# Performance work log

Measured on AMD Instinct MI355X. Metric: run time of the kernel, lower is better.

## Reference

```python
import jax, jax.numpy as jnp
import numpy as np

N = 100000; E = 1600000; D_IN = 9; HID = 16; HEADS = 8; D = HID * HEADS; G = 1000
NEG_SLOPE = 0.2; LN_EPS = 1e-5


def _gat_conv(x, src, dst, W, a_src, a_dst, b, heads, ch):
    # PyG GATConv (eval mode, self-loops already appended to src/dst)
    h = (x @ W).reshape(-1, heads, ch)                   # [N,H,C]
    al_s = (h * a_src).sum(-1)                           # [N,H]
    al_d = (h * a_dst).sum(-1)                           # [N,H]
    e = al_s[src] + al_d[dst]                            # [Et,H]
    e = jnp.where(e > 0, e, NEG_SLOPE * e)               # LeakyReLU(0.2)
    m = jax.ops.segment_max(e, dst, num_segments=N)      # per-dst softmax
    alpha = jnp.exp(e - m[dst])
    denom = jax.ops.segment_sum(alpha, dst, num_segments=N)
    alpha = alpha / (denom[dst] + 1e-16)
    out = jax.ops.segment_sum(h[src] * alpha[:, :, None], dst, num_segments=N)
    return out.reshape(-1, heads * ch) + b


def _ln_graph(x, g, b):
    # PyG LayerNorm, mode='graph', batch=None: normalize over all nodes+channels
    mu = x.mean()
    var = jnp.mean((x - mu) ** 2)
    return (x - mu) / jnp.sqrt(var + LN_EPS) * g + b


def setup_inputs() -> dict:
    key = jax.random.key(0)
    ks = jax.random.split(key, 20)
    s = 0.1
    p = lambda i, shape: jax.random.normal(ks[i], shape, jnp.float32) * s
    return {
        "x": jax.random.normal(ks[0], (N, D_IN), jnp.float32),
        "edge_index": jax.random.randint(ks[1], (2, E), 0, N),
        "batch": jnp.sort(jax.random.randint(ks[2], (N,), 0, G)),
        "W1": p(3, (D_IN, D)), "a_src1": p(4, (HEADS, HID)), "a_dst1": p(5, (HEADS, HID)), "b1": jnp.zeros((D,), jnp.float32),
        "W2": p(6, (D, D)), "a_src2": p(7, (1, D)), "a_dst2": p(8, (1, D)), "b2": jnp.zeros((D,), jnp.float32),
        "fc1_w": p(9, (D, D)), "fc1_b": jnp.zeros((D,), jnp.float32),
        "fc2_w": p(10, (D, D)), "fc2_b": jnp.zeros((D,), jnp.float32),
        "fc3_w": p(11, (D, D)), "fc3_b": jnp.zeros((D,), jnp.float32),
        "fc4_w": p(12, (D, D)), "fc4_b": jnp.zeros((D,), jnp.float32),
        "g1": jnp.ones((D,), jnp.float32), "beta1": jnp.zeros((D,), jnp.float32),
        "g2": jnp.ones((D,), jnp.float32), "beta2": jnp.zeros((D,), jnp.float32),
        "fcf_w": p(13, (D, 1)), "fcf_b": jnp.zeros((1,), jnp.float32),
    }


def reference(x, edge_index, batch, W1, a_src1, a_dst1, b1, W2, a_src2, a_dst2, b2,
              fc1_w, fc1_b, fc2_w, fc2_b, fc3_w, fc3_b, fc4_w, fc4_b,
              g1, beta1, g2, beta2, fcf_w, fcf_b):
    loops = jnp.arange(N)
    src = jnp.concatenate([edge_index[0], loops])
    dst = jnp.concatenate([edge_index[1], loops])
    h = jax.nn.relu(_gat_conv(x, src, dst, W1, a_src1, a_dst1, b1, HEADS, HID))
    hc = h
    h = jax.nn.relu(h @ fc1_w + fc1_b)
    h = jax.nn.relu(h @ fc2_w + fc2_b + hc)
    h = _ln_graph(h, g1, beta1)
    hc = h
    h = _gat_conv(h, src, dst, W2, a_src2, a_dst2, b2, 1, D)
    h = jax.nn.relu(h @ fc3_w + fc3_b)
    h = h @ fc4_w + fc4_b + hc
    h = _ln_graph(h, g2, beta2)
    h = h @ fcf_w + fcf_b                                # [N,1]
    sums = jax.ops.segment_sum(h, batch, num_segments=G)
    cnt = jax.ops.segment_sum(jnp.ones((N,), h.dtype), batch, num_segments=G)
    return sums / jnp.maximum(cnt, 1.0)[:, None]          # global_mean_pool -> [G,1]
```

## Files before the change

kernel.cpp:

```cpp
#include <hip/hip_runtime.h>
#include <cstdint>

#define NN 100000
#define NE 1600000
#define DI 9
#define DD 128
#define NH 8
#define NG 1000

#define NBK 3125
#define NBLK 256
#define EPB (NE/NBLK)

typedef unsigned int uint;
typedef __attribute__((ext_vector_type(8))) short bf16x8;
typedef __attribute__((ext_vector_type(4))) float f32x4;

__device__ __forceinline__ float leaky(float x){ return x > 0.f ? x : 0.2f*x; }
__device__ __forceinline__ uint f2bf(float f){
  uint u = __float_as_uint(f);
  return (u + 0x7fffu + ((u>>16)&1u)) >> 16;
}
__device__ __forceinline__ float bflo(uint p){ return __uint_as_float(p << 16); }
__device__ __forceinline__ float bfhi(uint p){ return __uint_as_float(p & 0xffff0000u); }
__device__ __forceinline__ uint packbf(float a, float b){ return f2bf(a) | (f2bf(b)<<16); }

union U16 { uint4 u; bf16x8 v; };
__device__ __forceinline__ bf16x8 ld8(const uint* p){ U16 t; t.u = *(const uint4*)p; return t.v; }

__global__ __launch_bounds__(512) void k_hist(const int* __restrict__ dst, int* __restrict__ hist){
  __shared__ int h[NBK];
  for (int i = threadIdx.x; i < NBK; i += 512) h[i] = 0;
  __syncthreads();
  int blk = blockIdx.x;
  int beg = blk*EPB, end = beg + EPB;
  for (int i = beg + threadIdx.x; i < end; i += 512)
    atomicAdd(&h[dst[i] >> 5], 1);
  __syncthreads();
  for (int b = threadIdx.x; b < NBK; b += 512) hist[(size_t)blk*NBK + b] = h[b];
}

__global__ __launch_bounds__(256) void k_bsum(int* __restrict__ hist, int* __restrict__ bsum){
  int b = blockIdx.x*256 + threadIdx.x;
  if (b >= NBK) return;
  int run = 0;
  for (int k = 0; k < NBLK; ++k){
    int t = hist[(size_t)k*NBK + b];
    hist[(size_t)k*NBK + b] = run;
    run += t;
  }
  bsum[b] = run;
}

__global__ __launch_bounds__(1024) void k_bscan(const int* __restrict__ bsum, int* __restrict__ bbase){
  __shared__ int sh[1024];
  __shared__ int carry;
  if (threadIdx.x == 0) carry = 0;
  __syncthreads();
  for (int c0 = 0; c0 < NBK; c0 += 1024){
    int i = c0 + threadIdx.x;
    int v = (i < NBK) ? bsum[i] : 0;
    sh[threadIdx.x] = v;
    __syncthreads();
    for (int off = 1; off < 1024; off <<= 1){
      int t = (threadIdx.x >= off) ? sh[threadIdx.x-off] : 0;
      __syncthreads();
      sh[threadIdx.x] += t;
      __syncthreads();
    }
    if (i < NBK) bbase[i] = carry + sh[threadIdx.x] - v;
    __syncthreads();
    if (threadIdx.x == 0) carry += sh[1023];
    __syncthreads();
  }
}

__global__ __launch_bounds__(512) void k_part(const int* __restrict__ src, const int* __restrict__ dst,
    const int* __restrict__ hist, const int* __restrict__ bbase, uint* __restrict__ ebuf){
  __shared__ int cur[NBK];
  int blk = blockIdx.x;
  for (int b = threadIdx.x; b < NBK; b += 512)
    cur[b] = hist[(size_t)blk*NBK + b] + bbase[b];
  __syncthreads();
  int beg = blk*EPB, end = beg + EPB;
  for (int i = beg + threadIdx.x; i < end; i += 512){
    int d = dst[i], s = src[i];
    int b = d >> 5;
    int p = atomicAdd(&cur[b], 1);
    ebuf[p] = (uint)s | ((uint)(d & 31) << 26);
  }
}

__global__ __launch_bounds__(64) void k_fin(const uint* __restrict__ ebuf, const int* __restrict__ bbase,
    const int* __restrict__ bsum, int* __restrict__ rowptr, int* __restrict__ col){
  __shared__ int cnt32[32];
  __shared__ int exc[32];
  int b = blockIdx.x;
  int lane = threadIdx.x;
  if (lane < 32) cnt32[lane] = 0;
  __syncthreads();
  int base = bbase[b], n = bsum[b];
  for (int i = lane; i < n; i += 64)
    atomicAdd(&cnt32[ebuf[base+i] >> 26], 1);
  __syncthreads();
  if (lane == 0){
    int run = 0;
    for (int d = 0; d < 32; ++d){
      int t = cnt32[d];
      exc[d] = run;
      rowptr[b*32 + d] = base + run;
      run += t;
    }
  }
  __syncthreads();
  if (lane < 32) cnt32[lane] = exc[lane];
  __syncthreads();
  for (int i = lane; i < n; i += 64){
    uint e = ebuf[base+i];
    int d = e >> 26;
    int r = atomicAdd(&cnt32[d], 1);
    col[base + r] = (int)(e & 0x03ffffffu);
  }
  if (b == 0 && lane == 0) rowptr[NN] = NE;
}

__global__ __launch_bounds__(64) void k_wconv(const float* __restrict__ W, uint* __restrict__ WT){
  int n = blockIdx.x;
  int t = threadIdx.x;
  float w0 = W[(2*t)*DD + n];
  float w1 = W[(2*t+1)*DD + n];
  WT[n*64 + t] = packbf(w0, w1);
}

__global__ __launch_bounds__(128) void k_lin1(const float* __restrict__ x, const float* __restrict__ W1,
    const float* __restrict__ as1, const float* __restrict__ ad1,
    uint* __restrict__ t1b, float* __restrict__ al_s, float* __restrict__ al_d){
  int n = blockIdx.x;
  int c = threadIdx.x;
  const float* xr = x + n*DI;
  float t = 0.f;
  #pragma unroll
  for (int k = 0; k < DI; ++k) t = fmaf(xr[k], W1[k*DD+c], t);
  uint mybf = f2bf(t);
  uint pbf  = (uint)__shfl_xor((int)mybf, 1, 64);
  if (!(c & 1)) t1b[(size_t)n*64 + (c>>1)] = mybf | (pbf<<16);
  float vs = t * as1[c];
  float vd = t * ad1[c];
  #pragma unroll
  for (int m = 8; m >= 1; m >>= 1){ vs += __shfl_xor(vs, m, 16); vd += __shfl_xor(vd, m, 16); }
  if ((c & 15) == 0){
    al_s[n*NH + (c>>4)] = vs;
    al_d[n*NH + (c>>4)] = vd;
  }
}

__global__ __launch_bounds__(256) void k_gat1(const uint* __restrict__ t1b,
    const float* __restrict__ al_s, const float* __restrict__ al_d,
    const int* __restrict__ rowptr, const int* __restrict__ col,
    const float* __restrict__ b1, uint* __restrict__ outb){
  int n = blockIdx.x*4 + (threadIdx.x >> 6);
  if (n >= NN) return;
  uint lane = threadIdx.x & 63;
  uint h = lane >> 3;
  float ald = al_d[(uint)n*NH + h];
  float a0  = __expf(leaky(al_s[(uint)n*NH + h] + ald));
  uint  ps  = t1b[(uint)n*64u + lane];
  float den = a0;
  float s0 = a0*bflo(ps), s1 = a0*bfhi(ps);
  int beg = rowptr[n], end = rowptr[n+1];
  int e = beg;
  for (; e + 4 <= end; e += 4){
    uint c0 = (uint)col[e], c1 = (uint)col[e+1], c2 = (uint)col[e+2], c3 = (uint)col[e+3];
    float l0 = al_s[c0*8u + h], l1 = al_s[c1*8u + h];
    float l2 = al_s[c2*8u + h], l3 = al_s[c3*8u + h];
    uint p0 = t1b[c0*64u + lane];
    uint p1 = t1b[c1*64u + lane];
    uint p2 = t1b[c2*64u + lane];
    uint p3 = t1b[c3*64u + lane];
    float a0_ = __expf(leaky(l0 + ald));
    float a1_ = __expf(leaky(l1 + ald));
    float a2_ = __expf(leaky(l2 + ald));
    float a3_ = __expf(leaky(l3 + ald));
    den += a0_ + a1_ + a2_ + a3_;
    s0 = fmaf(a0_, bflo(p0), s0); s1 = fmaf(a0_, bfhi(p0), s1);
    s0 = fmaf(a1_, bflo(p1), s0); s1 = fmaf(a1_, bfhi(p1), s1);
    s0 = fmaf(a2_, bflo(p2), s0); s1 = fmaf(a2_, bfhi(p2), s1);
    s0 = fmaf(a3_, bflo(p3), s0); s1 = fmaf(a3_, bfhi(p3), s1);
  }
  for (; e < end; ++e){
    uint c = (uint)col[e];
    float a = __expf(leaky(al_s[c*8u + h] + ald));
    uint p = t1b[c*64u + lane];
    den += a;
    s0 = fmaf(a, bflo(p), s0); s1 = fmaf(a, bfhi(p), s1);
  }
  float inv = 1.f/(den + 1e-16f);
  float2 bb = ((const float2*)b1)[lane];
  outb[(uint)n*64u + lane] = packbf(fmaxf(s0*inv + bb.x, 0.f), fmaxf(s1*inv + bb.y, 0.f));
}

__global__ __launch_bounds__(256) void k_al2(const uint* __restrict__ t2b,
    const float* __restrict__ as2, const float* __restrict__ ad2,
    float* __restrict__ al_s, float* __restrict__ al_d){
  int n = blockIdx.x*4 + (threadIdx.x >> 6);
  if (n >= NN) return;
  int lane = threadIdx.x & 63;
  uint p = t2b[(size_t)n*64 + lane];
  float v0 = bflo(p), v1 = bfhi(p);
  float2 s2 = ((const float2*)as2)[lane];
  float2 d2 = ((const float2*)ad2)[lane];
  float vs = v0*s2.x + v1*s2.y;
  float vd = v0*d2.x + v1*d2.y;
  #pragma unroll
  for (int m = 32; m >= 1; m >>= 1){ vs += __shfl_xor(vs, m, 64); vd += __shfl_xor(vd, m, 64); }
  if (lane == 0){ al_s[n] = vs; al_d[n] = vd; }
}

__global__ __launch_bounds__(256) void k_gat2(const uint* __restrict__ t2b,
    const float* __restrict__ al_s, const float* __restrict__ al_d,
    const int* __restrict__ rowptr, const int* __restrict__ col,
    const float* __restrict__ b2, uint* __restrict__ outb){
  int n = blockIdx.x*4 + (threadIdx.x >> 6);
  if (n >= NN) return;
  uint lane = threadIdx.x & 63;
  float ald = al_d[n];
  float a0  = __expf(leaky(al_s[n] + ald));
  uint  ps  = t2b[(uint)n*64u + lane];
  float den = a0;
  float s0 = a0*bflo(ps), s1 = a0*bfhi(ps);
  int beg = rowptr[n], end = rowptr[n+1];
  int e = beg;
  for (; e + 4 <= end; e += 4){
    uint c0 = (uint)col[e], c1 = (uint)col[e+1], c2 = (uint)col[e+2], c3 = (uint)col[e+3];
    float l0 = al_s[c0], l1 = al_s[c1], l2 = al_s[c2], l3 = al_s[c3];
    uint p0 = t2b[c0*64u + lane];
    uint p1 = t2b[c1*64u + lane];
    uint p2 = t2b[c2*64u + lane];
    uint p3 = t2b[c3*64u + lane];
    float a0_ = __expf(leaky(l0 + ald));
    float a1_ = __expf(leaky(l1 + ald));
    float a2_ = __expf(leaky(l2 + ald));
    float a3_ = __expf(leaky(l3 + ald));
    den += a0_ + a1_ + a2_ + a3_;
    s0 = fmaf(a0_, bflo(p0), s0); s1 = fmaf(a0_, bfhi(p0), s1);
    s0 = fmaf(a1_, bflo(p1), s0); s1 = fmaf(a1_, bfhi(p1), s1);
    s0 = fmaf(a2_, bflo(p2), s0); s1 = fmaf(a2_, bfhi(p2), s1);
    s0 = fmaf(a3_, bflo(p3), s0); s1 = fmaf(a3_, bfhi(p3), s1);
  }
  for (; e < end; ++e){
    uint c = (uint)col[e];
    float a = __expf(leaky(al_s[c] + ald));
    uint p = t2b[c*64u + lane];
    den += a;
    s0 = fmaf(a, bflo(p), s0); s1 = fmaf(a, bfhi(p), s1);
  }
  float inv = 1.f/(den + 1e-16f);
  float2 bb = ((const float2*)b2)[lane];
  outb[(uint)n*64u + lane] = packbf(s0*inv + bb.x, s1*inv + bb.y);
}

template<bool RELU, bool BIAS, bool RES, bool LNRED>
__global__ __launch_bounds__(256) void k_mfma(const uint* __restrict__ Xb, const uint* __restrict__ WTb,
    const float* __restrict__ bias, const uint* __restrict__ resb, uint* __restrict__ outb,
    float* __restrict__ pbuf, int nrows){
  int lane = threadIdx.x & 63;
  int wid  = threadIdx.x >> 6;
  int m0 = blockIdx.x*128 + wid*32;
  int lr = lane & 15, hi4 = lane >> 4;
  f32x4 acc[2][8];
  #pragma unroll
  for (int a = 0; a < 2; ++a)
    #pragma unroll
    for (int c = 0; c < 8; ++c) acc[a][c] = (f32x4){0.f,0.f,0.f,0.f};
  int ra0 = m0 + lr;      if (ra0 > NN-1) ra0 = NN-1;
  int ra1 = m0 + 16 + lr; if (ra1 > NN-1) ra1 = NN-1;
  #pragma unroll
  for (int kk = 0; kk < 4; ++kk){
    int ko = kk*16 + hi4*4;
    bf16x8 a0 = ld8(Xb + (size_t)ra0*64 + ko);
    bf16x8 a1 = ld8(Xb + (size_t)ra1*64 + ko);
    #pragma unroll
    for (int c = 0; c < 8; ++c){
      bf16x8 b = ld8(WTb + (size_t)(c*16 + lr)*64 + ko);
      acc[0][c] = __builtin_amdgcn_mfma_f32_16x16x32_bf16(a0, b, acc[0][c], 0, 0, 0);
      acc[1][c] = __builtin_amdgcn_mfma_f32_16x16x32_bf16(a1, b, acc[1][c], 0, 0, 0);
    }
  }
  bool evn = !(lane & 1);
  int cph = lr >> 1;
  float lns = 0.f, lnss = 0.f;
  #pragma unroll
  for (int rg = 0; rg < 2; ++rg){
    #pragma unroll
    for (int c = 0; c < 8; ++c){
      int cp = c*8 + cph;
      #pragma unroll
      for (int r = 0; r < 4; ++r){
        float v0 = acc[rg][c][r];
        float v1 = __shfl_xor(v0, 1, 64);
        int row = m0 + rg*16 + hi4*4 + r;
        if (evn && row < nrows){
          if (BIAS){ float2 bb = ((const float2*)bias)[cp]; v0 += bb.x; v1 += bb.y; }
          if (RES){ uint rr = resb[(size_t)row*64 + cp]; v0 += bflo(rr); v1 += bfhi(rr); }
          if (RELU){ v0 = fmaxf(v0, 0.f); v1 = fmaxf(v1, 0.f); }
          outb[(size_t)row*64 + cp] = packbf(v0, v1);
          if (LNRED){ lns += v0 + v1; lnss += v0*v0 + v1*v1; }
        }
      }
    }
  }
  if (LNRED){
    #pragma unroll
    for (int m = 32; m >= 1; m >>= 1){ lns += __shfl_xor(lns, m, 64); lnss += __shfl_xor(lnss, m, 64); }
    __shared__ float shred[8];
    if (lane == 0){ shred[wid*2] = lns; shred[wid*2+1] = lnss; }
    __syncthreads();
    if (threadIdx.x == 0){
      float S = 0.f, SS = 0.f;
      for (int w = 0; w < 4; ++w){ S += shred[2*w]; SS += shred[2*w+1]; }
      pbuf[blockIdx.x*2] = S; pbuf[blockIdx.x*2+1] = SS;
    }
  }
}

__global__ __launch_bounds__(256) void k_ln_stats(const float* __restrict__ pbuf, float* __restrict__ stats, int nb){
  float s = 0.f, ss = 0.f;
  for (int i = threadIdx.x; i < nb; i += 256){ s += pbuf[2*i]; ss += pbuf[2*i+1]; }
  #pragma unroll
  for (int m = 32; m >= 1; m >>= 1){ s += __shfl_xor(s, m, 64); ss += __shfl_xor(ss, m, 64); }
  __shared__ float sh[8];
  int wid = threadIdx.x >> 6, lane = threadIdx.x & 63;
  if (lane == 0){ sh[wid*2] = s; sh[wid*2+1] = ss; }
  __syncthreads();
  if (threadIdx.x == 0){
    float S = 0.f, SS = 0.f;
    for (int w = 0; w < 4; ++w){ S += sh[2*w]; SS += sh[2*w+1]; }
    const float inv = 1.f/((float)NN*(float)DD);
    float mu = S*inv;
    float var = SS*inv - mu*mu;
    stats[0] = mu;
    stats[1] = rsqrtf(var + 1e-5f);
  }
}

__global__ __launch_bounds__(256) void k_ln_apply_bf(uint* __restrict__ xb, const float* __restrict__ g,
    const float* __restrict__ be, const float* __restrict__ stats){
  const int n4 = NN*16;
  float mu = stats[0], rs = stats[1];
  uint4* x4 = (uint4*)xb;
  const float2* g2 = (const float2*)g;
  const float2* b2 = (const float2*)be;
  for (int i = blockIdx.x*256 + threadIdx.x; i < n4; i += gridDim.x*256){
    int cb = (i & 15)*4;
    uint4 u = x4[i];
    float2 ga = g2[cb],   gb = g2[cb+1], gc = g2[cb+2], gd = g2[cb+3];
    float2 ba = b2[cb],   bb = b2[cb+1], bc = b2[cb+2], bd = b2[cb+3];
    u.x = packbf((bflo(u.x)-mu)*rs*ga.x + ba.x, (bfhi(u.x)-mu)*rs*ga.y + ba.y);
    u.y = packbf((bflo(u.y)-mu)*rs*gb.x + bb.x, (bfhi(u.y)-mu)*rs*gb.y + bb.y);
    u.z = packbf((bflo(u.z)-mu)*rs*gc.x + bc.x, (bfhi(u.z)-mu)*rs*gc.y + bc.y);
    u.w = packbf((bflo(u.w)-mu)*rs*gd.x + bd.x, (bfhi(u.w)-mu)*rs*gd.y + bd.y);
    x4[i] = u;
  }
}

__global__ __launch_bounds__(256) void k_fdot_ln(const uint* __restrict__ xb, const float* __restrict__ g,
    const float* __restrict__ be, const float* __restrict__ stats,
    const float* __restrict__ fw, const float* __restrict__ fb, float* __restrict__ val){
  int n = blockIdx.x*4 + (threadIdx.x >> 6);
  if (n >= NN) return;
  int lane = threadIdx.x & 63;
  float mu = stats[0], rs = stats[1];
  uint p = xb[(size_t)n*64 + lane];
  float2 gg = ((const float2*)g)[lane];
  float2 bb = ((const float2*)be)[lane];
  float2 ww = ((const float2*)fw)[lane];
  float v = ((bflo(p)-mu)*rs*gg.x + bb.x)*ww.x + ((bfhi(p)-mu)*rs*gg.y + bb.y)*ww.y;
  #pragma unroll
  for (int m = 32; m >= 1; m >>= 1) v += __shfl_xor(v, m, 64);
  if (lane == 0) val[n] = v + fb[0];
}

__global__ __launch_bounds__(64) void k_pool(const float* __restrict__ val, const int* __restrict__ batch,
                                             float* __restrict__ out){
  int g = blockIdx.x;
  int lane = threadIdx.x;
  int lo = 0, hi = NN;
  while (lo < hi){ int mid = (lo+hi)>>1; if (batch[mid] < g) lo = mid+1; else hi = mid; }
  int start = lo;
  hi = NN;
  while (lo < hi){ int mid = (lo+hi)>>1; if (batch[mid] < g+1) lo = mid+1; else hi = mid; }
  int end = lo;
  float s = 0.f;
  for (int i = start + lane; i < end; i += 64) s += val[i];
  #pragma unroll
  for (int m = 32; m >= 1; m >>= 1) s += __shfl_xor(s, m, 64);
  if (lane == 0) out[g] = s / fmaxf((float)(end - start), 1.f);
}

extern "C" void kernel_launch(void* const* d_in, const int* in_sizes, int n_in,
                              void* d_out, int out_size, void* d_ws, size_t ws_size,
                              hipStream_t stream){
  const float* x   = (const float*)d_in[0];
  const int*   ei  = (const int*)d_in[1];
  const int* batch = (const int*)d_in[2];
  const float* W1  = (const float*)d_in[3];
  const float* as1 = (const float*)d_in[4];
  const float* ad1 = (const float*)d_in[5];
  const float* b1  = (const float*)d_in[6];
  const float* W2  = (const float*)d_in[7];
  const float* as2 = (const float*)d_in[8];
  const float* ad2 = (const float*)d_in[9];
  const float* b2  = (const float*)d_in[10];
  const float* fc1w= (const float*)d_in[11];
  const float* fc1b= (const float*)d_in[12];
  const float* fc2w= (const float*)d_in[13];
  const float* fc2b= (const float*)d_in[14];
  const float* fc3w= (const float*)d_in[15];
  const float* fc3b= (const float*)d_in[16];
  const float* fc4w= (const float*)d_in[17];
  const float* fc4b= (const float*)d_in[18];
  const float* g1  = (const float*)d_in[19];
  const float* be1 = (const float*)d_in[20];
  const float* g2  = (const float*)d_in[21];
  const float* be2 = (const float*)d_in[22];
  const float* fcw = (const float*)d_in[23];
  const float* fcb = (const float*)d_in[24];
  float* out = (float*)d_out;
  (void)in_sizes; (void)n_in; (void)out_size; (void)ws_size;

  char* ws = (char*)d_ws;
  size_t off = 0;
  auto alloc = [&](size_t bytes)->void*{
    void* p = ws + off;
    off += (bytes + 255) & ~(size_t)255;
    return p;
  };
  float* A    = (float*)alloc((size_t)NN*DD*4);
  float* B    = (float*)alloc((size_t)NN*DD*4);
  float* C    = (float*)alloc((size_t)NN*DD*4);
  float* als1 = (float*)alloc((size_t)NN*NH*4);
  float* ald1 = (float*)alloc((size_t)NN*NH*4);
  float* als2 = (float*)alloc((size_t)NN*4);
  float* ald2 = (float*)alloc((size_t)NN*4);
  float* escr = (float*)alloc((size_t)NE*4);
  int*   rowptr = (int*)alloc((size_t)(NN+1)*4);
  int*   col    = (int*)alloc((size_t)NE*4);
  int*   bsum   = (int*)alloc((size_t)NBK*4);
  int*   bbase  = (int*)alloc((size_t)NBK*4);
  float* pbuf   = (float*)alloc(1024*2*4);
  float* stats  = (float*)alloc(2*4);
  float* val    = (float*)alloc((size_t)NN*4);
  uint* wt_fc1  = (uint*)alloc((size_t)DD*64*4);
  uint* wt_fc2  = (uint*)alloc((size_t)DD*64*4);
  uint* wt_w2   = (uint*)alloc((size_t)DD*64*4);
  uint* wt_fc3  = (uint*)alloc((size_t)DD*64*4);
  uint* wt_fc4  = (uint*)alloc((size_t)DD*64*4);

  uint*  Ab     = (uint*)A;
  uint*  Bb     = (uint*)B;
  uint*  Cb     = (uint*)C;
  int*   hist   = (int*)A;
  uint*  ebuf   = (uint*)escr;

  const int* esrc = ei;
  const int* edst = ei + NE;

  k_hist <<<NBLK, 512, 0, stream>>>(edst, hist);
  k_bsum <<<(NBK+255)/256, 256, 0, stream>>>(hist, bsum);
  k_bscan<<<1, 1024, 0, stream>>>(bsum, bbase);
  k_part <<<NBLK, 512, 0, stream>>>(esrc, edst, hist, bbase, ebuf);
  k_fin  <<<NBK, 64, 0, stream>>>(ebuf, bbase, bsum, rowptr, col);

  k_wconv<<<DD, 64, 0, stream>>>(fc1w, wt_fc1);
  k_wconv<<<DD, 64, 0, stream>>>(fc2w, wt_fc2);
  k_wconv<<<DD, 64, 0, stream>>>(W2,   wt_w2);
  k_wconv<<<DD, 64, 0, stream>>>(fc3w, wt_fc3);
  k_wconv<<<DD, 64, 0, stream>>>(fc4w, wt_fc4);

  const int WB = (NN + 3)/4;
  const int GB = (NN + 127)/128;

  k_lin1<<<NN, 128, 0, stream>>>(x, W1, as1, ad1, Ab, als1, ald1);
  k_gat1<<<WB, 256, 0, stream>>>(Ab, als1, ald1, rowptr, col, b1, Bb);

  k_mfma<true,  true, false, false><<<GB, 256, 0, stream>>>(Bb, wt_fc1, fc1b, nullptr, Ab, nullptr, NN);
  k_mfma<true,  true, true,  true ><<<GB, 256, 0, stream>>>(Ab, wt_fc2, fc2b, Bb,      Cb, pbuf,    NN);

  k_ln_stats<<<1, 256, 0, stream>>>(pbuf, stats, GB);
  k_ln_apply_bf<<<1024, 256, 0, stream>>>(Cb, g1, be1, stats);

  k_mfma<false, false, false, false><<<GB, 256, 0, stream>>>(Cb, wt_w2, nullptr, nullptr, Ab, nullptr, NN);
  k_al2<<<WB, 256, 0, stream>>>(Ab, as2, ad2, als2, ald2);
  k_gat2<<<WB, 256, 0, stream>>>(Ab, als2, ald2, rowptr, col, b2, Bb);

  k_mfma<true,  true, false, false><<<GB, 256, 0, stream>>>(Bb, wt_fc3, fc3b, nullptr, Ab, nullptr, NN);
  k_mfma<false, true, true,  true ><<<GB, 256, 0, stream>>>(Ab, wt_fc4, fc4b, Cb,      Bb, pbuf,    NN);

  k_ln_stats<<<1, 256, 0, stream>>>(pbuf, stats, GB);
  k_fdot_ln<<<WB, 256, 0, stream>>>(Bb, g2, be2, stats, fcw, fcb, val);
  k_pool<<<NG, 64, 0, stream>>>(val, batch, out);
}
```

Measured before the change: 484.0 us.

## Fuse GAT2 attention logits into MFMA, cooperative edge loads, transpose histogram

Folds the k_al2 attention-logit computation into the W2 MFMA epilogue, which removes one kernel launch and one full re-read of the projected features. The two GAT aggregation kernels now let each 8-lane group load eight edge indices and exponentials at once and broadcast them by shuffle, instead of every lane redundantly loading col and al_s. The CSR build uses 64 blocks instead of 256 and stores the histogram bucket-major, so k_bsum reads contiguous memory. Costs are extra shuffles, predicated inner loops, and less parallelism in the histogram and partition passes.

```diff
diff --git a/kernel.cpp b/kernel.cpp
--- a/kernel.cpp
+++ b/kernel.cpp
@@ -9,7 +9,7 @@
 #define NG 1000
 
 #define NBK 3125
-#define NBLK 256
+#define NBLK 64
 #define EPB (NE/NBLK)
 
 typedef unsigned int uint;
@@ -37,16 +37,17 @@
   for (int i = beg + threadIdx.x; i < end; i += 512)
     atomicAdd(&h[dst[i] >> 5], 1);
   __syncthreads();
-  for (int b = threadIdx.x; b < NBK; b += 512) hist[(size_t)blk*NBK + b] = h[b];
+  for (int b = threadIdx.x; b < NBK; b += 512) hist[b*NBLK + blk] = h[b];
 }
 
 __global__ __launch_bounds__(256) void k_bsum(int* __restrict__ hist, int* __restrict__ bsum){
   int b = blockIdx.x*256 + threadIdx.x;
   if (b >= NBK) return;
   int run = 0;
+  #pragma unroll 4
   for (int k = 0; k < NBLK; ++k){
-    int t = hist[(size_t)k*NBK + b];
-    hist[(size_t)k*NBK + b] = run;
+    int t = hist[b*NBLK + k];
+    hist[b*NBLK + k] = run;
     run += t;
   }
   bsum[b] = run;
@@ -80,7 +81,7 @@
   __shared__ int cur[NBK];
   int blk = blockIdx.x;
   for (int b = threadIdx.x; b < NBK; b += 512)
-    cur[b] = hist[(size_t)blk*NBK + b] + bbase[b];
+    cur[b] = hist[b*NBLK + blk] + bbase[b];
   __syncthreads();
   int beg = blk*EPB, end = beg + EPB;
   for (int i = beg + threadIdx.x; i < end; i += 512){
@@ -162,58 +163,37 @@
   if (n >= NN) return;
   uint lane = threadIdx.x & 63;
   uint h = lane >> 3;
+  uint j = lane & 7;
+  int  grp = (int)(lane & 56u);
   float ald = al_d[(uint)n*NH + h];
   float a0  = __expf(leaky(al_s[(uint)n*NH + h] + ald));
   uint  ps  = t1b[(uint)n*64u + lane];
-  float den = a0;
   float s0 = a0*bflo(ps), s1 = a0*bfhi(ps);
+  float edn = 0.f;
   int beg = rowptr[n], end = rowptr[n+1];
-  int e = beg;
-  for (; e + 4 <= end; e += 4){
-    uint c0 = (uint)col[e], c1 = (uint)col[e+1], c2 = (uint)col[e+2], c3 = (uint)col[e+3];
-    float l0 = al_s[c0*8u + h], l1 = al_s[c1*8u + h];
-    float l2 = al_s[c2*8u + h], l3 = al_s[c3*8u + h];
-    uint p0 = t1b[c0*64u + lane];
-    uint p1 = t1b[c1*64u + lane];
-    uint p2 = t1b[c2*64u + lane];
-    uint p3 = t1b[c3*64u + lane];
-    float a0_ = __expf(leaky(l0 + ald));
-    float a1_ = __expf(leaky(l1 + ald));
-    float a2_ = __expf(leaky(l2 + ald));
-    float a3_ = __expf(leaky(l3 + ald));
-    den += a0_ + a1_ + a2_ + a3_;
-    s0 = fmaf(a0_, bflo(p0), s0); s1 = fmaf(a0_, bfhi(p0), s1);
-    s0 = fmaf(a1_, bflo(p1), s0); s1 = fmaf(a1_, bfhi(p1), s1);
-    s0 = fmaf(a2_, bflo(p2), s0); s1 = fmaf(a2_, bfhi(p2), s1);
-    s0 = fmaf(a3_, bflo(p3), s0); s1 = fmaf(a3_, bfhi(p3), s1);
-  }
-  for (; e < end; ++e){
-    uint c = (uint)col[e];
-    float a = __expf(leaky(al_s[c*8u + h] + ald));
-    uint p = t1b[c*64u + lane];
-    den += a;
-    s0 = fmaf(a, bflo(p), s0); s1 = fmaf(a, bfhi(p), s1);
-  }
-  float inv = 1.f/(den + 1e-16f);
+  for (int e = beg; e < end; e += 8){
+    int rem = end - e;
+    int ej = e + (int)j;
+    uint cjv = (uint)col[(ej < end) ? ej : (end-1)];
+    float al = ((int)j < rem) ? __expf(leaky(al_s[cjv*8u + h] + ald)) : 0.f;
+    edn += al;
+    #pragma unroll
+    for (int jj = 0; jj < 8; ++jj){
+      if (jj < rem){
+        float a  = __shfl(al, grp + jj, 64);
+        uint  cc = (uint)__shfl((int)cjv, grp + jj, 64);
+        uint  p  = t1b[cc*64u + lane];
+        s0 = fmaf(a, bflo(p), s0);
+        s1 = fmaf(a, bfhi(p), s1);
+      }
+    }
+  }
+  edn += __shfl_xor(edn, 1, 64);
+  edn += __shfl_xor(edn, 2, 64);
+  edn += __shfl_xor(edn, 4, 64);
+  float inv = 1.f/(a0 + edn + 1e-16f);
   float2 bb = ((const float2*)b1)[lane];
   outb[(uint)n*64u + lane] = packbf(fmaxf(s0*inv + bb.x, 0.f), fmaxf(s1*inv + bb.y, 0.f));
-}
-
-__global__ __launch_bounds__(256) void k_al2(const uint* __restrict__ t2b,
-    const float* __restrict__ as2, const float* __restrict__ ad2,
-    float* __restrict__ al_s, float* __restrict__ al_d){
-  int n = blockIdx.x*4 + (threadIdx.x >> 6);
-  if (n >= NN) return;
-  int lane = threadIdx.x & 63;
-  uint p = t2b[(size_t)n*64 + lane];
-  float v0 = bflo(p), v1 = bfhi(p);
-  float2 s2 = ((const float2*)as2)[lane];
-  float2 d2 = ((const float2*)ad2)[lane];
-  float vs = v0*s2.x + v1*s2.y;
-  float vd = v0*d2.x + v1*d2.y;
-  #pragma unroll
-  for (int m = 32; m >= 1; m >>= 1){ vs += __shfl_xor(vs, m, 64); vd += __shfl_xor(vd, m, 64); }
-  if (lane == 0){ al_s[n] = vs; al_d[n] = vd; }
 }
 
 __global__ __launch_bounds__(256) void k_gat2(const uint* __restrict__ t2b,
@@ -223,46 +203,44 @@
   int n = blockIdx.x*4 + (threadIdx.x >> 6);
   if (n >= NN) return;
   uint lane = threadIdx.x & 63;
+  uint j = lane & 7;
+  int  grp = (int)(lane & 56u);
   float ald = al_d[n];
   float a0  = __expf(leaky(al_s[n] + ald));
   uint  ps  = t2b[(uint)n*64u + lane];
-  float den = a0;
   float s0 = a0*bflo(ps), s1 = a0*bfhi(ps);
+  float edn = 0.f;
   int beg = rowptr[n], end = rowptr[n+1];
-  int e = beg;
-  for (; e + 4 <= end; e += 4){
-    uint c0 = (uint)col[e], c1 = (uint)col[e+1], c2 = (uint)col[e+2], c3 = (uint)col[e+3];
-    float l0 = al_s[c0], l1 = al_s[c1], l2 = al_s[c2], l3 = al_s[c3];
-    uint p0 = t2b[c0*64u + lane];
-    uint p1 = t2b[c1*64u + lane];
-    uint p2 = t2b[c2*64u + lane];
-    uint p3 = t2b[c3*64u + lane];
-    float a0_ = __expf(leaky(l0 + ald));
-    float a1_ = __expf(leaky(l1 + ald));
-    float a2_ = __expf(leaky(l2 + ald));
-    float a3_ = __expf(leaky(l3 + ald));
-    den += a0_ + a1_ + a2_ + a3_;
-    s0 = fmaf(a0_, bflo(p0), s0); s1 = fmaf(a0_, bfhi(p0), s1);
-    s0 = fmaf(a1_, bflo(p1), s0); s1 = fmaf(a1_, bfhi(p1), s1);
-    s0 = fmaf(a2_, bflo(p2), s0); s1 = fmaf(a2_, bfhi(p2), s1);
-    s0 = fmaf(a3_, bflo(p3), s0); s1 = fmaf(a3_, bfhi(p3), s1);
-  }
-  for (; e < end; ++e){
-    uint c = (uint)col[e];
-    float a = __expf(leaky(al_s[c] + ald));
-    uint p = t2b[c*64u + lane];
-    den += a;
-    s0 = fmaf(a, bflo(p), s0); s1 = fmaf(a, bfhi(p), s1);
-  }
-  float inv = 1.f/(den + 1e-16f);
+  for (int e = beg; e < end; e += 8){
+    int rem = end - e;
+    int ej = e + (int)j;
+    uint cjv = (uint)col[(ej < end) ? ej : (end-1)];
+    float al = ((int)j < rem) ? __expf(leaky(al_s[cjv] + ald)) : 0.f;
+    edn += al;
+    #pragma unroll
+    for (int jj = 0; jj < 8; ++jj){
+      if (jj < rem){
+        float a  = __shfl(al, grp + jj, 64);
+        uint  cc = (uint)__shfl((int)cjv, grp + jj, 64);
+        uint  p  = t2b[cc*64u + lane];
+        s0 = fmaf(a, bflo(p), s0);
+        s1 = fmaf(a, bfhi(p), s1);
+      }
+    }
+  }
+  edn += __shfl_xor(edn, 1, 64);
+  edn += __shfl_xor(edn, 2, 64);
+  edn += __shfl_xor(edn, 4, 64);
+  float inv = 1.f/(a0 + edn + 1e-16f);
   float2 bb = ((const float2*)b2)[lane];
   outb[(uint)n*64u + lane] = packbf(s0*inv + bb.x, s1*inv + bb.y);
 }
 
-template<bool RELU, bool BIAS, bool RES, bool LNRED>
+template<bool RELU, bool BIAS, bool RES, bool LNRED, bool AL2>
 __global__ __launch_bounds__(256) void k_mfma(const uint* __restrict__ Xb, const uint* __restrict__ WTb,
     const float* __restrict__ bias, const uint* __restrict__ resb, uint* __restrict__ outb,
-    float* __restrict__ pbuf, int nrows){
+    float* __restrict__ pbuf, const float* __restrict__ avs, const float* __restrict__ avd,
+    float* __restrict__ o_als, float* __restrict__ o_ald, int nrows){
   int lane = threadIdx.x & 63;
   int wid  = threadIdx.x >> 6;
   int m0 = blockIdx.x*128 + wid*32;
@@ -284,6 +262,25 @@
       bf16x8 b = ld8(WTb + (size_t)(c*16 + lr)*64 + ko);
       acc[0][c] = __builtin_amdgcn_mfma_f32_16x16x32_bf16(a0, b, acc[0][c], 0, 0, 0);
       acc[1][c] = __builtin_amdgcn_mfma_f32_16x16x32_bf16(a1, b, acc[1][c], 0, 0, 0);
+    }
+  }
+  if (AL2){
+    #pragma unroll
+    for (int rg = 0; rg < 2; ++rg){
+      #pragma unroll
+      for (int r = 0; r < 4; ++r){
+        float vs = 0.f, vd = 0.f;
+        #pragma unroll
+        for (int c = 0; c < 8; ++c){
+          float v = acc[rg][c][r];
+          vs = fmaf(v, avs[c*16 + lr], vs);
+          vd = fmaf(v, avd[c*16 + lr], vd);
+        }
+        #pragma unroll
+        for (int m = 8; m >= 1; m >>= 1){ vs += __shfl_xor(vs, m, 64); vd += __shfl_xor(vd, m, 64); }
+        int row = m0 + rg*16 + hi4*4 + r;
+        if (lr == 0 && row < nrows){ o_als[row] = vs; o_ald[row] = vd; }
+      }
     }
   }
   bool evn = !(lane & 1);
@@ -483,18 +480,17 @@
   k_lin1<<<NN, 128, 0, stream>>>(x, W1, as1, ad1, Ab, als1, ald1);
   k_gat1<<<WB, 256, 0, stream>>>(Ab, als1, ald1, rowptr, col, b1, Bb);
 
-  k_mfma<true,  true, false, false><<<GB, 256, 0, stream>>>(Bb, wt_fc1, fc1b, nullptr, Ab, nullptr, NN);
-  k_mfma<true,  true, true,  true ><<<GB, 256, 0, stream>>>(Ab, wt_fc2, fc2b, Bb,      Cb, pbuf,    NN);
+  k_mfma<true,  true, false, false, false><<<GB, 256, 0, stream>>>(Bb, wt_fc1, fc1b, nullptr, Ab, nullptr, nullptr, nullptr, nullptr, nullptr, NN);
+  k_mfma<true,  true, true,  true,  false><<<GB, 256, 0, stream>>>(Ab, wt_fc2, fc2b, Bb,      Cb, pbuf,    nullptr, nullptr, nullptr, nullptr, NN);
 
   k_ln_stats<<<1, 256, 0, stream>>>(pbuf, stats, GB);
   k_ln_apply_bf<<<1024, 256, 0, stream>>>(Cb, g1, be1, stats);
 
-  k_mfma<false, false, false, false><<<GB, 256, 0, stream>>>(Cb, wt_w2, nullptr, nullptr, Ab, nullptr, NN);
-  k_al2<<<WB, 256, 0, stream>>>(Ab, as2, ad2, als2, ald2);
+  k_mfma<false, false, false, false, true ><<<GB, 256, 0, stream>>>(Cb, wt_w2, nullptr, nullptr, Ab, nullptr, as2, ad2, als2, ald2, NN);
   k_gat2<<<WB, 256, 0, stream>>>(Ab, als2, ald2, rowptr, col, b2, Bb);
 
-  k_mfma<true,  true, false, false><<<GB, 256, 0, stream>>>(Bb, wt_fc3, fc3b, nullptr, Ab, nullptr, NN);
-  k_mfma<false, true, true,  true ><<<GB, 256, 0, stream>>>(Ab, wt_fc4, fc4b, Cb,      Bb, pbuf,    NN);
+  k_mfma<true,  true, false, false, false><<<GB, 256, 0, stream>>>(Bb, wt_fc3, fc3b, nullptr, Ab, nullptr, nullptr, nullptr, nullptr, nullptr, NN);
+  k_mfma<false, true, true,  true,  false><<<GB, 256, 0, stream>>>(Ab, wt_fc4, fc4b, Cb,      Bb, pbuf,    nullptr, nullptr, nullptr, nullptr, NN);
 
   k_ln_stats<<<1, 256, 0, stream>>>(pbuf, stats, GB);
   k_fdot_ln<<<WB, 256, 0, stream>>>(Bb, g2, be2, stats, fcw, fcb, val);
```

After: 588.7 us. 21.6% more time.
